# Kernel optimization log

Hardware: AMD Instinct MI355X
Metric: run time of the kernel (lower is better)

The kernel has to match this reference:

```python
import jax, jax.numpy as jnp
import numpy as np

EMBED_DIM = 1024
NUM_HEADS = 16
D_K = EMBED_DIM // NUM_HEADS
B, S = 2, 2048


def setup_inputs() -> dict:
    key = jax.random.key(0)
    kq, kk, kv = jax.random.split(key, 3)
    q = jax.random.normal(kq, (B, S, EMBED_DIM), dtype=jnp.float32)
    k = jax.random.normal(kk, (B, S, EMBED_DIM), dtype=jnp.float32)
    v = jax.random.normal(kv, (B, S, EMBED_DIM), dtype=jnp.float32)
    # causal mask, broadcast over batch and heads; 0 entries are masked out
    mask = jnp.tril(jnp.ones((S, S), dtype=jnp.int32))[None, None, :, :]
    return {"q": q, "k": k, "v": v, "mask": mask}


def _separate_heads(x):
    b, s, _ = x.shape
    return x.reshape(b, s, NUM_HEADS, D_K).transpose(0, 2, 1, 3)  # [b,h,s,d]


def reference(q, k, v, mask):
    qh = _separate_heads(q)
    kh = _separate_heads(k)
    vh = _separate_heads(v)
    # scores: [b, h, s_q, s_k]
    scores = jnp.einsum("bhqd,bhkd->bhqk", qh, kh) / jnp.sqrt(jnp.float32(D_K))
    scores = jnp.where(mask == 0, jnp.float32(-1e9), scores)
    attn = jax.nn.softmax(scores, axis=-1)  # dropout is identity in eval mode
    out = jnp.einsum("bhqk,bhkd->bhqd", attn, vh)
    out = out.transpose(0, 2, 1, 3).reshape(q.shape)
    return out, attn
```

## Files before the change

kernel.cpp:

```cpp
#include <hip/hip_runtime.h>
#include <cstdint>
#include <cstddef>


#define SLEN 2048
#define EMB  1024
#define DK   64
#define BK   128

typedef __attribute__((ext_vector_type(8))) short short8;
typedef __attribute__((ext_vector_type(4))) float floatx4;
typedef __attribute__((ext_vector_type(4))) short short4v;
typedef __attribute__((ext_vector_type(2))) short short2v;

__device__ __forceinline__ short f2bf(float f) {
    union { float f; unsigned u; } c; c.f = f;
    unsigned u = c.u + 0x7fffu + ((c.u >> 16) & 1u);
    return (short)(u >> 16);
}
__device__ __forceinline__ float bf2f(short s) {
    union { unsigned u; float f; } c;
    c.u = ((unsigned)(unsigned short)s) << 16;
    return c.f;
}

#define KS_LD 72
#define VT_LD 136
#define PS_LD 136

__device__ __forceinline__ void decode_block(int g, int& bh, int& j, int& half) {
    half = g & 1;
    j    = (g >> 1) & 7;
    bh   = g >> 4;
}

__device__ __forceinline__ void load_q_frags(const float* __restrict__ Q, int b, int h,
                                             int grow, int quad, short8* aq ) {
    const float* qp = Q + (size_t)(b * SLEN + grow) * EMB + h * DK;
#pragma unroll
    for (int ch = 0; ch < 2; ++ch) {
        const float4* p4 = (const float4*)(qp + ch * 32 + quad * 8);
        float4 x0 = p4[0], x1 = p4[1];
        short8 a;
        a[0] = f2bf(x0.x * 0.125f); a[1] = f2bf(x0.y * 0.125f);
        a[2] = f2bf(x0.z * 0.125f); a[3] = f2bf(x0.w * 0.125f);
        a[4] = f2bf(x1.x * 0.125f); a[5] = f2bf(x1.y * 0.125f);
        a[6] = f2bf(x1.z * 0.125f); a[7] = f2bf(x1.w * 0.125f);
        aq[ch] = a;
    }
}

__device__ __forceinline__ void stage_k(const float* __restrict__ K, int b, int h,
                                        int k0, int t, short* Ks) {
    const int col = (t & 15) * 4;
    const int rb  = t >> 4;
#pragma unroll
    for (int p = 0; p < 8; ++p) {
        const int row = p * 16 + rb;
        const float4 x = *(const float4*)(K + (size_t)(b * SLEN + k0 + row) * EMB + h * DK + col);
        short4v s;
        s[0] = f2bf(x.x); s[1] = f2bf(x.y); s[2] = f2bf(x.z); s[3] = f2bf(x.w);
        *(short4v*)&Ks[row * KS_LD + col] = s;
    }
}

__global__ __launch_bounds__(256, 4)
void rowsum_kernel(const float* __restrict__ Q, const float* __restrict__ K,
                   float* __restrict__ invbuf)
{
    __shared__ short Ks[BK * KS_LD];

    int bh, j, half; decode_block(blockIdx.x, bh, j, half);
    const int b = bh >> 4, h = bh & 15;
    const int qt[2]    = { j, 15 - j };
    const int qbase[2] = { qt[0] * 128 + half * 64, qt[1] * 128 + half * 64 };

    const int t    = threadIdx.x;
    const int w    = t >> 6;
    const int lane = t & 63;
    const int quad = lane >> 4;
    const int l15  = lane & 15;

    short8 aq[2][2];
    load_q_frags(Q, b, h, qbase[0] + w * 16 + l15, quad, aq[0]);
    load_q_frags(Q, b, h, qbase[1] + w * 16 + l15, quad, aq[1]);

    float rs[2][4];
#pragma unroll
    for (int qh = 0; qh < 2; ++qh)
#pragma unroll
        for (int r = 0; r < 4; ++r) rs[qh][r] = 0.f;

    const int ktmax = 15 - j;
    for (int kt = 0; kt <= ktmax; ++kt) {
        const int k0 = kt * BK;
        __syncthreads();
        stage_k(K, b, h, k0, t, Ks);
        __syncthreads();
#pragma unroll
        for (int n = 0; n < 8; ++n) {
            const short8 b0 = *(const short8*)&Ks[(n * 16 + l15) * KS_LD + quad * 8];
            const short8 b1 = *(const short8*)&Ks[(n * 16 + l15) * KS_LD + 32 + quad * 8];
            const int colg = k0 + n * 16 + l15;
#pragma unroll
            for (int qh = 0; qh < 2; ++qh) {
                if (qh == 0 && kt > j) continue;
                floatx4 c = {0.f, 0.f, 0.f, 0.f};
                c = __builtin_amdgcn_mfma_f32_16x16x32_bf16(aq[qh][0], b0, c, 0, 0, 0);
                c = __builtin_amdgcn_mfma_f32_16x16x32_bf16(aq[qh][1], b1, c, 0, 0, 0);
                const int rowg = qbase[qh] + w * 16 + quad * 4;
                const bool diag = (kt == qt[qh]);
#pragma unroll
                for (int r = 0; r < 4; ++r) {
                    const float p = (!diag || (colg <= rowg + r)) ? __expf(c[r]) : 0.f;
                    rs[qh][r] += p;
                }
            }
        }
    }

#pragma unroll
    for (int qh = 0; qh < 2; ++qh)
#pragma unroll
        for (int r = 0; r < 4; ++r) {
            float v = rs[qh][r];
            v += __shfl_xor(v, 1);
            v += __shfl_xor(v, 2);
            v += __shfl_xor(v, 4);
            v += __shfl_xor(v, 8);
            if (l15 == 0)
                invbuf[(size_t)bh * SLEN + qbase[qh] + w * 16 + quad * 4 + r] = 1.0f / v;
        }
}

__global__ __launch_bounds__(256, 3)
void attn_main_kernel(const float* __restrict__ Q, const float* __restrict__ K,
                      const float* __restrict__ V, const float* __restrict__ invbuf,
                      float* __restrict__ out, float* __restrict__ attn)
{
    __shared__ short Ks[BK * KS_LD];
    __shared__ short Vt[DK * VT_LD];
    __shared__ short Ps[64 * PS_LD];

    int bh, j, half; decode_block(blockIdx.x, bh, j, half);
    const int b = bh >> 4, h = bh & 15;
    const int qt[2]    = { j, 15 - j };
    const int qbase[2] = { qt[0] * 128 + half * 64, qt[1] * 128 + half * 64 };

    const int t    = threadIdx.x;
    const int w    = t >> 6;
    const int lane = t & 63;
    const int quad = lane >> 4;
    const int l15  = lane & 15;

    short8 aq[2][2];
    load_q_frags(Q, b, h, qbase[0] + w * 16 + l15, quad, aq[0]);
    load_q_frags(Q, b, h, qbase[1] + w * 16 + l15, quad, aq[1]);

    float invr[2][4];
#pragma unroll
    for (int qh = 0; qh < 2; ++qh)
#pragma unroll
        for (int r = 0; r < 4; ++r)
            invr[qh][r] = invbuf[(size_t)bh * SLEN + qbase[qh] + w * 16 + quad * 4 + r];

    floatx4 o[2][4];
#pragma unroll
    for (int qh = 0; qh < 2; ++qh)
#pragma unroll
        for (int n = 0; n < 4; ++n) o[qh][n] = (floatx4){0.f, 0.f, 0.f, 0.f};

    float* const attn_bh = attn + (size_t)bh * SLEN * SLEN;

    const int ktmax = 15 - j;
    for (int kt = 0; kt <= ktmax; ++kt) {
        const int k0 = kt * BK;
        stage_k(K, b, h, k0, t, Ks);
        {
            const int kp = t & 63;
            const int dg = t >> 6;
#pragma unroll
            for (int p = 0; p < 4; ++p) {
                const int db = p * 16 + dg * 4;
                const float* vb = V + (size_t)(b * SLEN + k0 + 2 * kp) * EMB + h * DK + db;
                const float4 x0 = *(const float4*)vb;
                const float4 x1 = *(const float4*)(vb + EMB);
                short2v s;
                s[0] = f2bf(x0.x); s[1] = f2bf(x1.x); *(short2v*)&Vt[(db + 0) * VT_LD + 2 * kp] = s;
                s[0] = f2bf(x0.y); s[1] = f2bf(x1.y); *(short2v*)&Vt[(db + 1) * VT_LD + 2 * kp] = s;
                s[0] = f2bf(x0.z); s[1] = f2bf(x1.z); *(short2v*)&Vt[(db + 2) * VT_LD + 2 * kp] = s;
                s[0] = f2bf(x0.w); s[1] = f2bf(x1.w); *(short2v*)&Vt[(db + 3) * VT_LD + 2 * kp] = s;
            }
        }
        __syncthreads();

#pragma unroll
        for (int qh = 0; qh < 2; ++qh) {
            if (qh == 0 && kt > j) continue;
            const bool diag = (kt == qt[qh]);
#pragma unroll
            for (int n = 0; n < 8; ++n) {
                const short8 b0 = *(const short8*)&Ks[(n * 16 + l15) * KS_LD + quad * 8];
                const short8 b1 = *(const short8*)&Ks[(n * 16 + l15) * KS_LD + 32 + quad * 8];
                const int colg = k0 + n * 16 + l15;
                floatx4 c = {0.f, 0.f, 0.f, 0.f};
                c = __builtin_amdgcn_mfma_f32_16x16x32_bf16(aq[qh][0], b0, c, 0, 0, 0);
                c = __builtin_amdgcn_mfma_f32_16x16x32_bf16(aq[qh][1], b1, c, 0, 0, 0);
                const int rowl = w * 16 + quad * 4;
                const int rowg = qbase[qh] + rowl;
#pragma unroll
                for (int r = 0; r < 4; ++r) {
                    const float p = (!diag || (colg <= rowg + r))
                                        ? __expf(c[r]) * invr[qh][r] : 0.f;
                    Ps[(rowl + r) * PS_LD + n * 16 + l15] = f2bf(p);
                }
            }
            __syncthreads();
            {
                const int c4 = (t & 31) * 4;
                const int rb = t >> 5;
#pragma unroll
                for (int i = 0; i < 8; ++i) {
                    const int row = i * 8 + rb;
                    const short4v pv = *(const short4v*)&Ps[row * PS_LD + c4];
                    float4 f;
                    f.x = bf2f(pv[0]); f.y = bf2f(pv[1]); f.z = bf2f(pv[2]); f.w = bf2f(pv[3]);
                    *(float4*)(attn_bh + (size_t)(qbase[qh] + row) * SLEN + k0 + c4) = f;
                }
            }
#pragma unroll
            for (int ch = 0; ch < 4; ++ch) {
                const short8 ap = *(const short8*)&Ps[(w * 16 + l15) * PS_LD + ch * 32 + quad * 8];
#pragma unroll
                for (int n = 0; n < 4; ++n) {
                    const short8 bv = *(const short8*)&Vt[(n * 16 + l15) * VT_LD + ch * 32 + quad * 8];
                    o[qh][n] = __builtin_amdgcn_mfma_f32_16x16x32_bf16(ap, bv, o[qh][n], 0, 0, 0);
                }
            }
            __syncthreads();
        }
    }

#pragma unroll
    for (int qh = 0; qh < 2; ++qh) {
        const int rowg = qbase[qh] + w * 16 + quad * 4;
#pragma unroll
        for (int n = 0; n < 4; ++n) {
            const int col = h * DK + n * 16 + l15;
#pragma unroll
            for (int r = 0; r < 4; ++r)
                out[(size_t)(b * SLEN + rowg + r) * EMB + col] = o[qh][n][r];
        }
    }

    const float4 z = {0.f, 0.f, 0.f, 0.f};
#pragma unroll
    for (int qh = 0; qh < 2; ++qh) {
        const int z0 = (qt[qh] + 1) * BK;
        if (z0 >= SLEN) continue;
        for (int row = w; row < 64; row += 4) {
            float* rp = attn_bh + (size_t)(qbase[qh] + row) * SLEN;
            for (int c = z0 + lane * 4; c < SLEN; c += 256)
                *(float4*)(rp + c) = z;
        }
    }
}

extern "C" void kernel_launch(void* const* d_in, const int* in_sizes, int n_in,
                              void* d_out, int out_size, void* d_ws, size_t ws_size,
                              hipStream_t stream) {
    const float* Q = (const float*)d_in[0];
    const float* K = (const float*)d_in[1];
    const float* V = (const float*)d_in[2];
    float* out    = (float*)d_out;
    float* attn   = out + (size_t)2 * SLEN * EMB;
    float* invbuf = (float*)d_ws;

    rowsum_kernel<<<dim3(512), dim3(256), 0, stream>>>(Q, K, invbuf);
    attn_main_kernel<<<dim3(512), dim3(256), 0, stream>>>(Q, K, V, invbuf, out, attn);
}
```

Before: 738.8 us.

## Fuse rowsum and main attention kernels with register prefetch and interleaved zero-fill

Merges the row-sum pass and the main attention pass into one kernel, so the softmax normalisers stay in registers and the workspace round-trip and second launch go away. Global loads of the next K/V tile are prefetched into registers while the current tile is computed. The zero-fill of the masked attention region is spread across loop iterations instead of done in a tail loop. The cost is higher register pressure (launch bounds lowered to 2 blocks per CU), which reduces occupancy.

```diff
diff --git a/kernel.cpp b/kernel.cpp
--- a/kernel.cpp
+++ b/kernel.cpp
@@ -28,50 +28,20 @@
 #define VT_LD 136
 #define PS_LD 136
 
-__device__ __forceinline__ void decode_block(int g, int& bh, int& j, int& half) {
-    half = g & 1;
-    j    = (g >> 1) & 7;
-    bh   = g >> 4;
-}
-
-__device__ __forceinline__ void load_q_frags(const float* __restrict__ Q, int b, int h,
-                                             int grow, int quad, short8* aq ) {
-    const float* qp = Q + (size_t)(b * SLEN + grow) * EMB + h * DK;
-#pragma unroll
-    for (int ch = 0; ch < 2; ++ch) {
-        const float4* p4 = (const float4*)(qp + ch * 32 + quad * 8);
-        float4 x0 = p4[0], x1 = p4[1];
-        short8 a;
-        a[0] = f2bf(x0.x * 0.125f); a[1] = f2bf(x0.y * 0.125f);
-        a[2] = f2bf(x0.z * 0.125f); a[3] = f2bf(x0.w * 0.125f);
-        a[4] = f2bf(x1.x * 0.125f); a[5] = f2bf(x1.y * 0.125f);
-        a[6] = f2bf(x1.z * 0.125f); a[7] = f2bf(x1.w * 0.125f);
-        aq[ch] = a;
-    }
-}
-
-__device__ __forceinline__ void stage_k(const float* __restrict__ K, int b, int h,
-                                        int k0, int t, short* Ks) {
-    const int col = (t & 15) * 4;
-    const int rb  = t >> 4;
-#pragma unroll
-    for (int p = 0; p < 8; ++p) {
-        const int row = p * 16 + rb;
-        const float4 x = *(const float4*)(K + (size_t)(b * SLEN + k0 + row) * EMB + h * DK + col);
-        short4v s;
-        s[0] = f2bf(x.x); s[1] = f2bf(x.y); s[2] = f2bf(x.z); s[3] = f2bf(x.w);
-        *(short4v*)&Ks[row * KS_LD + col] = s;
-    }
-}
-
-__global__ __launch_bounds__(256, 4)
-void rowsum_kernel(const float* __restrict__ Q, const float* __restrict__ K,
-                   float* __restrict__ invbuf)
+__global__ __launch_bounds__(256, 2)
+void attn_fused_kernel(const float* __restrict__ Q, const float* __restrict__ K,
+                       const float* __restrict__ V, float* __restrict__ out,
+                       float* __restrict__ attn)
 {
     __shared__ short Ks[BK * KS_LD];
-
-    int bh, j, half; decode_block(blockIdx.x, bh, j, half);
-    const int b = bh >> 4, h = bh & 15;
+    __shared__ short Vt[DK * VT_LD];
+    __shared__ short Ps[64 * PS_LD];
+
+    const int g    = blockIdx.x;
+    const int half = g & 1;
+    const int j    = (g >> 1) & 7;
+    const int bh   = g >> 4;
+    const int b    = bh >> 4, h = bh & 15;
     const int qt[2]    = { j, 15 - j };
     const int qbase[2] = { qt[0] * 128 + half * 64, qt[1] * 128 + half * 64 };
 
@@ -81,9 +51,29 @@
     const int quad = lane >> 4;
     const int l15  = lane & 15;
 
+    const int kcol = (t & 15) * 4;
+    const int krb  = t >> 4;
+    const int vkp  = t & 63;
+    const int vdg  = t >> 6;
+
     short8 aq[2][2];
-    load_q_frags(Q, b, h, qbase[0] + w * 16 + l15, quad, aq[0]);
-    load_q_frags(Q, b, h, qbase[1] + w * 16 + l15, quad, aq[1]);
+#pragma unroll
+    for (int qh = 0; qh < 2; ++qh) {
+        const float* qp = Q + (size_t)(b * SLEN + qbase[qh] + w * 16 + l15) * EMB + h * DK;
+#pragma unroll
+        for (int ch = 0; ch < 2; ++ch) {
+            const float4* p4 = (const float4*)(qp + ch * 32 + quad * 8);
+            float4 x0 = p4[0], x1 = p4[1];
+            short8 a;
+            a[0] = f2bf(x0.x * 0.125f); a[1] = f2bf(x0.y * 0.125f);
+            a[2] = f2bf(x0.z * 0.125f); a[3] = f2bf(x0.w * 0.125f);
+            a[4] = f2bf(x1.x * 0.125f); a[5] = f2bf(x1.y * 0.125f);
+            a[6] = f2bf(x1.z * 0.125f); a[7] = f2bf(x1.w * 0.125f);
+            aq[qh][ch] = a;
+        }
+    }
+
+    const int ktmax = 15 - j;
 
     float rs[2][4];
 #pragma unroll
@@ -91,12 +81,27 @@
 #pragma unroll
         for (int r = 0; r < 4; ++r) rs[qh][r] = 0.f;
 
-    const int ktmax = 15 - j;
+    float4 kpre[8];
+#pragma unroll
+    for (int p = 0; p < 8; ++p)
+        kpre[p] = *(const float4*)(K + (size_t)(b * SLEN + p * 16 + krb) * EMB + h * DK + kcol);
+
     for (int kt = 0; kt <= ktmax; ++kt) {
+#pragma unroll
+        for (int p = 0; p < 8; ++p) {
+            short4v s;
+            s[0] = f2bf(kpre[p].x); s[1] = f2bf(kpre[p].y);
+            s[2] = f2bf(kpre[p].z); s[3] = f2bf(kpre[p].w);
+            *(short4v*)&Ks[(p * 16 + krb) * KS_LD + kcol] = s;
+        }
+        __syncthreads();
+        if (kt < ktmax) {
+            const int k0n = (kt + 1) * BK;
+#pragma unroll
+            for (int p = 0; p < 8; ++p)
+                kpre[p] = *(const float4*)(K + (size_t)(b * SLEN + k0n + p * 16 + krb) * EMB + h * DK + kcol);
+        }
         const int k0 = kt * BK;
-        __syncthreads();
-        stage_k(K, b, h, k0, t, Ks);
-        __syncthreads();
 #pragma unroll
         for (int n = 0; n < 8; ++n) {
             const short8 b0 = *(const short8*)&Ks[(n * 16 + l15) * KS_LD + quad * 8];
@@ -117,8 +122,10 @@
                 }
             }
         }
-    }
-
+        __syncthreads();
+    }
+
+    float invr[2][4];
 #pragma unroll
     for (int qh = 0; qh < 2; ++qh)
 #pragma unroll
@@ -128,71 +135,60 @@
             v += __shfl_xor(v, 2);
             v += __shfl_xor(v, 4);
             v += __shfl_xor(v, 8);
-            if (l15 == 0)
-                invbuf[(size_t)bh * SLEN + qbase[qh] + w * 16 + quad * 4 + r] = 1.0f / v;
-        }
-}
-
-__global__ __launch_bounds__(256, 3)
-void attn_main_kernel(const float* __restrict__ Q, const float* __restrict__ K,
-                      const float* __restrict__ V, const float* __restrict__ invbuf,
-                      float* __restrict__ out, float* __restrict__ attn)
-{
-    __shared__ short Ks[BK * KS_LD];
-    __shared__ short Vt[DK * VT_LD];
-    __shared__ short Ps[64 * PS_LD];
-
-    int bh, j, half; decode_block(blockIdx.x, bh, j, half);
-    const int b = bh >> 4, h = bh & 15;
-    const int qt[2]    = { j, 15 - j };
-    const int qbase[2] = { qt[0] * 128 + half * 64, qt[1] * 128 + half * 64 };
-
-    const int t    = threadIdx.x;
-    const int w    = t >> 6;
-    const int lane = t & 63;
-    const int quad = lane >> 4;
-    const int l15  = lane & 15;
-
-    short8 aq[2][2];
-    load_q_frags(Q, b, h, qbase[0] + w * 16 + l15, quad, aq[0]);
-    load_q_frags(Q, b, h, qbase[1] + w * 16 + l15, quad, aq[1]);
-
-    float invr[2][4];
+            invr[qh][r] = 1.0f / v;
+        }
+
+    floatx4 o[2][4];
 #pragma unroll
     for (int qh = 0; qh < 2; ++qh)
 #pragma unroll
-        for (int r = 0; r < 4; ++r)
-            invr[qh][r] = invbuf[(size_t)bh * SLEN + qbase[qh] + w * 16 + quad * 4 + r];
-
-    floatx4 o[2][4];
-#pragma unroll
-    for (int qh = 0; qh < 2; ++qh)
-#pragma unroll
         for (int n = 0; n < 4; ++n) o[qh][n] = (floatx4){0.f, 0.f, 0.f, 0.f};
 
     float* const attn_bh = attn + (size_t)bh * SLEN * SLEN;
 
-    const int ktmax = 15 - j;
+    float4 vpre[8];
+#pragma unroll
+    for (int p = 0; p < 8; ++p)
+        kpre[p] = *(const float4*)(K + (size_t)(b * SLEN + p * 16 + krb) * EMB + h * DK + kcol);
+#pragma unroll
+    for (int p = 0; p < 4; ++p) {
+        const float* vb = V + (size_t)(b * SLEN + 2 * vkp) * EMB + h * DK + p * 16 + vdg * 4;
+        vpre[2 * p]     = *(const float4*)vb;
+        vpre[2 * p + 1] = *(const float4*)(vb + EMB);
+    }
+
     for (int kt = 0; kt <= ktmax; ++kt) {
+#pragma unroll
+        for (int p = 0; p < 8; ++p) {
+            short4v s;
+            s[0] = f2bf(kpre[p].x); s[1] = f2bf(kpre[p].y);
+            s[2] = f2bf(kpre[p].z); s[3] = f2bf(kpre[p].w);
+            *(short4v*)&Ks[(p * 16 + krb) * KS_LD + kcol] = s;
+        }
+#pragma unroll
+        for (int p = 0; p < 4; ++p) {
+            const int db = p * 16 + vdg * 4;
+            const float4 x0 = vpre[2 * p], x1 = vpre[2 * p + 1];
+            short2v s;
+            s[0] = f2bf(x0.x); s[1] = f2bf(x1.x); *(short2v*)&Vt[(db + 0) * VT_LD + 2 * vkp] = s;
+            s[0] = f2bf(x0.y); s[1] = f2bf(x1.y); *(short2v*)&Vt[(db + 1) * VT_LD + 2 * vkp] = s;
+            s[0] = f2bf(x0.z); s[1] = f2bf(x1.z); *(short2v*)&Vt[(db + 2) * VT_LD + 2 * vkp] = s;
+            s[0] = f2bf(x0.w); s[1] = f2bf(x1.w); *(short2v*)&Vt[(db + 3) * VT_LD + 2 * vkp] = s;
+        }
+        __syncthreads();
+        if (kt < ktmax) {
+            const int k0n = (kt + 1) * BK;
+#pragma unroll
+            for (int p = 0; p < 8; ++p)
+                kpre[p] = *(const float4*)(K + (size_t)(b * SLEN + k0n + p * 16 + krb) * EMB + h * DK + kcol);
+#pragma unroll
+            for (int p = 0; p < 4; ++p) {
+                const float* vb = V + (size_t)(b * SLEN + k0n + 2 * vkp) * EMB + h * DK + p * 16 + vdg * 4;
+                vpre[2 * p]     = *(const float4*)vb;
+                vpre[2 * p + 1] = *(const float4*)(vb + EMB);
+            }
+        }
         const int k0 = kt * BK;
-        stage_k(K, b, h, k0, t, Ks);
-        {
-            const int kp = t & 63;
-            const int dg = t >> 6;
-#pragma unroll
-            for (int p = 0; p < 4; ++p) {
-                const int db = p * 16 + dg * 4;
-                const float* vb = V + (size_t)(b * SLEN + k0 + 2 * kp) * EMB + h * DK + db;
-                const float4 x0 = *(const float4*)vb;
-                const float4 x1 = *(const float4*)(vb + EMB);
-                short2v s;
-                s[0] = f2bf(x0.x); s[1] = f2bf(x1.x); *(short2v*)&Vt[(db + 0) * VT_LD + 2 * kp] = s;
-                s[0] = f2bf(x0.y); s[1] = f2bf(x1.y); *(short2v*)&Vt[(db + 1) * VT_LD + 2 * kp] = s;
-                s[0] = f2bf(x0.z); s[1] = f2bf(x1.z); *(short2v*)&Vt[(db + 2) * VT_LD + 2 * kp] = s;
-                s[0] = f2bf(x0.w); s[1] = f2bf(x1.w); *(short2v*)&Vt[(db + 3) * VT_LD + 2 * kp] = s;
-            }
-        }
-        __syncthreads();
 
 #pragma unroll
         for (int qh = 0; qh < 2; ++qh) {
@@ -239,6 +235,28 @@
             }
             __syncthreads();
         }
+
+        {
+            const int c4 = (t & 31) * 4;
+            const int rb = t >> 5;
+            const float4 z = {0.f, 0.f, 0.f, 0.f};
+            if (kt > j) {
+                float* base = attn_bh + (size_t)qbase[0] * SLEN + kt * BK;
+#pragma unroll
+                for (int i = 0; i < 8; ++i)
+                    *(float4*)(base + (size_t)(i * 8 + rb) * SLEN + c4) = z;
+            }
+            if (kt >= 1 && kt <= j) {
+                const int zt = 15 - j + kt;
+                float* base0 = attn_bh + (size_t)qbase[0] * SLEN + zt * BK;
+                float* base1 = attn_bh + (size_t)qbase[1] * SLEN + zt * BK;
+#pragma unroll
+                for (int i = 0; i < 8; ++i) {
+                    *(float4*)(base0 + (size_t)(i * 8 + rb) * SLEN + c4) = z;
+                    *(float4*)(base1 + (size_t)(i * 8 + rb) * SLEN + c4) = z;
+                }
+            }
+        }
     }
 
 #pragma unroll
@@ -250,18 +268,6 @@
 #pragma unroll
             for (int r = 0; r < 4; ++r)
                 out[(size_t)(b * SLEN + rowg + r) * EMB + col] = o[qh][n][r];
-        }
-    }
-
-    const float4 z = {0.f, 0.f, 0.f, 0.f};
-#pragma unroll
-    for (int qh = 0; qh < 2; ++qh) {
-        const int z0 = (qt[qh] + 1) * BK;
-        if (z0 >= SLEN) continue;
-        for (int row = w; row < 64; row += 4) {
-            float* rp = attn_bh + (size_t)(qbase[qh] + row) * SLEN;
-            for (int c = z0 + lane * 4; c < SLEN; c += 256)
-                *(float4*)(rp + c) = z;
         }
     }
 }
@@ -272,10 +278,7 @@
     const float* Q = (const float*)d_in[0];
     const float* K = (const float*)d_in[1];
     const float* V = (const float*)d_in[2];
-    float* out    = (float*)d_out;
-    float* attn   = out + (size_t)2 * SLEN * EMB;
-    float* invbuf = (float*)d_ws;
-
-    rowsum_kernel<<<dim3(512), dim3(256), 0, stream>>>(Q, K, invbuf);
-    attn_main_kernel<<<dim3(512), dim3(256), 0, stream>>>(Q, K, V, invbuf, out, attn);
-}
+    float* out  = (float*)d_out;
+    float* attn = out + (size_t)2 * SLEN * EMB;
+    attn_fused_kernel<<<dim3(512), dim3(256), 0, stream>>>(Q, K, V, out, attn);
+}
```

Result: faster. 652.5 us (-11.7%).
